# Kernel tuning notes

Measured on AMD Instinct MI355X. Metric: run time of the kernel, lower is better.

Reference implementation:

```python
import jax, jax.numpy as jnp
import numpy as np

B, N, C = 16, 2048, 80
CONF_THR = 0.2
NMS_THR = 0.45
OFFSET = 10000.0  # > max box coordinate, separates classes for batched per-class NMS


def setup_inputs() -> dict:
    key = jax.random.key(0)
    k1, k2, k3, k4 = jax.random.split(key, 4)
    cxcy = jax.random.uniform(k1, (B, N, 2)) * 640.0
    wh = jax.random.uniform(k2, (B, N, 2)) * 100.0 + 1.0
    boxes = jnp.concatenate([cxcy - wh / 2, cxcy + wh / 2], axis=-1)  # (x1,y1,x2,y2)
    scores = jax.random.uniform(k3, (B, N, 1))
    classprobs = jax.random.uniform(k4, (B, N, C))
    detection = jnp.concatenate([boxes, scores, classprobs], axis=-1)  # [B,N,85]
    return {"detection": detection}


def _iou_matrix(boxes):
    # boxes: [N,4] -> [N,N] pairwise IoU (torchvision convention, no +1)
    x1, y1, x2, y2 = boxes[:, 0], boxes[:, 1], boxes[:, 2], boxes[:, 3]
    area = jnp.clip(x2 - x1, 0.0) * jnp.clip(y2 - y1, 0.0)
    ix1 = jnp.maximum(x1[:, None], x1[None, :])
    iy1 = jnp.maximum(y1[:, None], y1[None, :])
    ix2 = jnp.minimum(x2[:, None], x2[None, :])
    iy2 = jnp.minimum(y2[:, None], y2[None, :])
    inter = jnp.clip(ix2 - ix1, 0.0) * jnp.clip(iy2 - iy1, 0.0)
    return inter / (area[:, None] + area[None, :] - inter + 1e-7)


def _filter_image(boxes, scores, classprobs, labels):
    # Confidence filter (target_class=None path)
    cand = scores > CONF_THR
    # Sort by descending score, non-candidates last (sort key is non-differentiable)
    sort_key = jnp.where(cand, scores, -jnp.inf)
    order = jnp.argsort(-jax.lax.stop_gradient(sort_key))
    b = boxes[order]
    s = scores[order]
    cp = classprobs[order]
    lb = labels[order]
    cd = cand[order]
    # Per-class NMS via coordinate offset: boxes of different classes never overlap
    ob = b + lb[:, None].astype(b.dtype) * OFFSET
    iou = _iou_matrix(ob)  # [N,N]
    idx = jnp.arange(N)

    def step(active, i):
        keep_i = active[i]
        active = active & ~(keep_i & (iou[i] > NMS_THR) & (idx > i))
        return active, keep_i

    _, keep = jax.lax.scan(step, cd, idx)
    # Final sort by descending score among kept boxes (max_predictions_per_image=-1)
    final_key = jnp.where(keep, jax.lax.stop_gradient(s), -jnp.inf)
    perm = jnp.argsort(-final_key)
    keep_p = keep[perm]
    m = keep_p.astype(b.dtype)
    out_boxes = b[perm] * m[:, None]
    out_scores = s[perm] * m
    out_classprobs = cp[perm] * m
    out_labels = jnp.where(keep_p, lb[perm], 0)
    return out_boxes, out_scores, out_classprobs, out_labels, keep_p


def reference(detection):
    # split_detections
    boxes = detection[..., :4]
    scores = detection[..., 4]
    cp_all = detection[..., 5:]
    classprobs = jnp.max(cp_all, axis=-1)
    labels = jnp.argmax(cp_all, axis=-1)
    ob, osc, ocp, olb, mask = jax.vmap(_filter_image)(boxes, scores, classprobs, labels)
    # Pack float outputs: [B, N, 6] = boxes(4) + score(1) + classprob(1); padded rows are zero
    out = jnp.concatenate([ob, osc[..., None], ocp[..., None]], axis=-1)
    return out, olb, mask
```

## Files before the change

### kernel.cpp

```cpp
#include <hip/hip_runtime.h>

#define BATCH 16
#define NBOX  2048
#define NCLS  80
#define ROWF  85
#define CONF_THRF 0.2f
#define CONF_BITS 0x3E4CCCCDu
#define NMS_THRF  0.45f
#define CAP   128
#define KCAP  64
#define JOBS  (BATCH*NCLS)

#define WS_SL   0
#define WS_CP   (WS_SL + (size_t)BATCH*NBOX*8)
#define WS_KC   (WS_CP + (size_t)BATCH*NBOX*4)
#define WS_KB   (WS_KC + (size_t)JOBS*KCAP*8)
#define WS_KCP  (WS_KB + (size_t)JOBS*KCAP*16)
#define WS_KCLS (WS_KCP + (size_t)JOBS*KCAP*4)

static __device__ inline unsigned long long shflx64(unsigned long long v, int m) {
  int lo = __shfl_xor((int)(unsigned)(v & 0xffffffffull), m, 64);
  int hi = __shfl_xor((int)(unsigned)(v >> 32), m, 64);
  return ((unsigned long long)(unsigned)hi << 32) | (unsigned)lo;
}

__global__ __launch_bounds__(256) void prep_kernel(const float* __restrict__ det,
                                                   unsigned long long* __restrict__ sl,
                                                   float* __restrict__ cp_ws,
                                                   float* __restrict__ outz) {
  const int tid = threadIdx.x;
  const int lane = tid & 63, wavei = tid >> 6;
  const int sub = lane & 15, grp = lane >> 4;
  const int row = blockIdx.x * 16 + wavei * 4 + grp;

  int gid = blockIdx.x * 256 + tid;
  if (gid < (BATCH * NBOX * 8) / 4)
    ((float4*)outz)[gid] = make_float4(0.f, 0.f, 0.f, 0.f);

  const float* r = det + (size_t)row * ROWF;
  float best = r[5 + sub];
  int bc = sub;
#pragma unroll
  for (int k = 1; k < 5; ++k) {
    float v = r[5 + sub + 16 * k];
    if (v > best) { best = v; bc = sub + 16 * k; }
  }
#pragma unroll
  for (int d = 1; d < 16; d <<= 1) {
    float ov = __shfl_xor(best, d, 16);
    int oc = __shfl_xor(bc, d, 16);
    if (ov > best || (ov == best && oc < bc)) { best = ov; bc = oc; }
  }
  if (sub == 0) {
    sl[row] = ((unsigned long long)__float_as_uint(r[4]) << 32) | (unsigned)bc;
    cp_ws[row] = best;
  }
}

__global__ __launch_bounds__(256) void nms16_kernel(const float* __restrict__ det,
                                                    const unsigned long long* __restrict__ sl,
                                                    const float* __restrict__ cp_ws,
                                                    unsigned long long* __restrict__ keptc,
                                                    float4* __restrict__ keptb,
                                                    float* __restrict__ keptcp,
                                                    int* __restrict__ kcls) {
  __shared__ unsigned short cand[4][CAP];
  const int tid = threadIdx.x;
  const int lane = tid & 63, wid = tid >> 6;
  const int j = blockIdx.x * 4 + wid;
  const int img = j / NCLS, c = j - img * NCLS;
  const size_t ibase = (size_t)img * NBOX;
  const unsigned long long* slImg = sl + ibase;
  unsigned short* mycand = cand[wid];

  unsigned mymask = 0;
#pragma unroll
  for (int it = 0; it < 32; ++it) {
    unsigned long long v = slImg[it * 64 + lane];
    bool match = ((unsigned)(v >> 32) > CONF_BITS) && ((unsigned)v == (unsigned)c);
    mymask |= (match ? 1u : 0u) << it;
  }
  int mycnt = __popc(mymask);
  int inc = mycnt;
#pragma unroll
  for (int d = 1; d < 64; d <<= 1) { int u = __shfl_up(inc, d, 64); if (lane >= d) inc += u; }
  int mybase = inc - mycnt;
  int total = __shfl(inc, 63, 64);
  int m = total < CAP ? total : CAP;
  {
    unsigned mk = mymask;
    int pos = mybase;
    while (mk) {
      int it = __ffs(mk) - 1; mk &= mk - 1;
      if (pos < CAP) mycand[pos] = (unsigned short)(it * 64 + lane);
      pos++;
    }
  }

  unsigned long long e0 = ~0ull, e1 = ~0ull;
  if (lane < m) {
    int n = mycand[lane];
    e0 = ((unsigned long long)(~(unsigned)(slImg[n] >> 32)) << 32) | (unsigned)n;
  }
  if (lane + 64 < m) {
    int n = mycand[lane + 64];
    e1 = ((unsigned long long)(~(unsigned)(slImg[n] >> 32)) << 32) | (unsigned)n;
  }
  const bool two = (m > 64);
  if (!two) {
#pragma unroll
    for (int k = 2; k <= 64; k <<= 1)
      for (int jj = k >> 1; jj > 0; jj >>= 1) {
        bool amLow = (lane & jj) == 0;
        bool up = ((lane & k) == 0);
        unsigned long long o = shflx64(e0, jj);
        e0 = (up == amLow) ? (e0 < o ? e0 : o) : (e0 > o ? e0 : o);
      }
  } else {
#pragma unroll
    for (int k = 2; k <= 128; k <<= 1)
      for (int jj = k >> 1; jj > 0; jj >>= 1) {
        if (jj == 64) {
          bool up = ((lane & k) == 0);
          if (up ? (e0 > e1) : (e0 < e1)) { unsigned long long t = e0; e0 = e1; e1 = t; }
        } else {
          bool amLow = (lane & jj) == 0;
          bool up0 = ((lane & k) == 0), up1 = (((lane + 64) & k) == 0);
          unsigned long long o0 = shflx64(e0, jj), o1 = shflx64(e1, jj);
          e0 = (up0 == amLow) ? (e0 < o0 ? e0 : o0) : (e0 > o0 ? e0 : o0);
          e1 = (up1 == amLow) ? (e1 < o1 ? e1 : o1) : (e1 > o1 ? e1 : o1);
        }
      }
  }

  const float off = (float)c * 10000.0f;
  bool valid0 = lane < m, valid1 = two && (lane + 64 < m);
  int n0 = (int)((unsigned)e0 & (NBOX - 1));
  int n1 = (int)((unsigned)e1 & (NBOX - 1));
  float a00 = 0, a01 = 0, a02 = 0, a03 = 0, cp0 = 0;
  float x1 = 0, y1 = 0, x2 = 0, y2 = 0, ar = 0;
  if (valid0) {
    const float* rr = det + (ibase + n0) * ROWF;
    a00 = rr[0]; a01 = rr[1]; a02 = rr[2]; a03 = rr[3];
    cp0 = cp_ws[ibase + n0];
    x1 = a00 + off; y1 = a01 + off; x2 = a02 + off; y2 = a03 + off;
    ar = fmaxf(x2 - x1, 0.0f) * fmaxf(y2 - y1, 0.0f);
  }
  float A10 = 0, A11 = 0, A12 = 0, A13 = 0, cp1 = 0;
  float X1 = 0, Y1 = 0, X2 = 0, Y2 = 0, AR = 0;
  if (valid1) {
    const float* rr = det + (ibase + n1) * ROWF;
    A10 = rr[0]; A11 = rr[1]; A12 = rr[2]; A13 = rr[3];
    cp1 = cp_ws[ibase + n1];
    X1 = A10 + off; Y1 = A11 + off; X2 = A12 + off; Y2 = A13 + off;
    AR = fmaxf(X2 - X1, 0.0f) * fmaxf(Y2 - Y1, 0.0f);
  }

  unsigned long long keptm0 = 0, und = __ballot(valid0);
  while (und) {
    int i = __ffsll((long long)und) - 1;
    keptm0 |= 1ull << i;
    float kx1 = __shfl(x1, i, 64), ky1 = __shfl(y1, i, 64);
    float kx2 = __shfl(x2, i, 64), ky2 = __shfl(y2, i, 64);
    float kar = __shfl(ar, i, 64);
    float iw = fminf(x2, kx2) - fmaxf(x1, kx1);
    float ih = fminf(y2, ky2) - fmaxf(y1, ky1);
    float inter = fmaxf(iw, 0.0f) * fmaxf(ih, 0.0f);
    float iou = inter / (((kar + ar) - inter) + 1e-7f);
    bool sup = (lane > i) && (iou > NMS_THRF);
    und &= ~__ballot(sup);
    und &= ~(1ull << i);
  }
  unsigned long long keptm1 = 0;
  if (two) {
    bool dead = false;
    unsigned long long km = keptm0;
    while (km) {
      int t = __ffsll((long long)km) - 1; km &= km - 1;
      float kx1 = __shfl(x1, t, 64), ky1 = __shfl(y1, t, 64);
      float kx2 = __shfl(x2, t, 64), ky2 = __shfl(y2, t, 64);
      float kar = __shfl(ar, t, 64);
      float iw = fminf(X2, kx2) - fmaxf(X1, kx1);
      float ih = fminf(Y2, ky2) - fmaxf(Y1, ky1);
      float inter = fmaxf(iw, 0.0f) * fmaxf(ih, 0.0f);
      float iou = inter / (((kar + AR) - inter) + 1e-7f);
      dead |= (iou > NMS_THRF);
    }
    unsigned long long und1 = __ballot(valid1 && !dead);
    while (und1) {
      int i = __ffsll((long long)und1) - 1;
      keptm1 |= 1ull << i;
      float kx1 = __shfl(X1, i, 64), ky1 = __shfl(Y1, i, 64);
      float kx2 = __shfl(X2, i, 64), ky2 = __shfl(Y2, i, 64);
      float kar = __shfl(AR, i, 64);
      float iw = fminf(X2, kx2) - fmaxf(X1, kx1);
      float ih = fminf(Y2, ky2) - fmaxf(Y1, ky1);
      float inter = fmaxf(iw, 0.0f) * fmaxf(ih, 0.0f);
      float iou = inter / (((kar + AR) - inter) + 1e-7f);
      bool sup = (lane > i) && (iou > NMS_THRF);
      und1 &= ~__ballot(sup);
      und1 &= ~(1ull << i);
    }
  }

  unsigned long long* dstk = keptc + (size_t)j * KCAP;
  float4* dstb = keptb + (size_t)j * KCAP;
  float* dstc = keptcp + (size_t)j * KCAP;
  if ((keptm0 >> lane) & 1) {
    int rank = __popcll(keptm0 & ((1ull << lane) - 1ull));
    if (rank < KCAP) {
      dstk[rank] = (e0 & 0xffffffff00000000ull) | (unsigned)((n0 << 7) | c);
      dstb[rank] = make_float4(a00, a01, a02, a03);
      dstc[rank] = cp0;
    }
  }
  if (two && ((keptm1 >> lane) & 1)) {
    int rank = __popcll(keptm0) + __popcll(keptm1 & ((1ull << lane) - 1ull));
    if (rank < KCAP) {
      dstk[rank] = (e1 & 0xffffffff00000000ull) | (unsigned)((n1 << 7) | c);
      dstb[rank] = make_float4(A10, A11, A12, A13);
      dstc[rank] = cp1;
    }
  }
  if (lane == 0) {
    int nk = __popcll(keptm0) + __popcll(keptm1);
    kcls[j] = nk < KCAP ? nk : KCAP;
  }
}

__global__ __launch_bounds__(1024) void outr_kernel(const float* __restrict__ cp_unused,
                                                    const unsigned long long* __restrict__ keptc,
                                                    const float4* __restrict__ keptb,
                                                    const float* __restrict__ keptcp,
                                                    const int* __restrict__ kcls,
                                                    float* __restrict__ out) {
  __shared__ unsigned long long keys[NBOX];
  __shared__ unsigned short srcmap[NBOX];
  __shared__ int offL[NCLS], cntL[NCLS];
  __shared__ int KtotS;
  const int img = blockIdx.x >> 5, seg = blockIdx.x & 31;
  const int tid = threadIdx.x;
  const int lane = tid & 63, wid = tid >> 6;
  const size_t ibase = (size_t)img * NBOX;

  if (wid == 0) {
    int v0 = kcls[img * NCLS + lane];
    int v1 = (lane < NCLS - 64) ? kcls[img * NCLS + 64 + lane] : 0;
    int s0 = v0;
#pragma unroll
    for (int d = 1; d < 64; d <<= 1) { int u = __shfl_up(s0, d, 64); if (lane >= d) s0 += u; }
    int total0 = __shfl(s0, 63, 64);
    int s1 = v1;
#pragma unroll
    for (int d = 1; d < 16; d <<= 1) { int u = __shfl_up(s1, d, 64); if (lane >= d) s1 += u; }
    offL[lane] = s0 - v0; cntL[lane] = v0;
    if (lane < NCLS - 64) { offL[64 + lane] = total0 + s1 - v1; cntL[64 + lane] = v1; }
    if (lane == 15) KtotS = total0 + s1;
  }
  __syncthreads();
  const int K = KtotS;
  if (seg * 64 >= K) return;

  {
    const int c = tid % NCLS;
    const int q0 = tid / NCLS;
    const int step = (c < (1024 - NCLS * (1024 / NCLS))) ? (1024 / NCLS + 1) : (1024 / NCLS);
    int kc = cntL[c], o = offL[c];
    const unsigned long long* srck = keptc + (size_t)(img * NCLS + c) * KCAP;
    for (int q = q0; q < kc; q += step) {
      keys[o + q] = srck[q];
      srcmap[o + q] = (unsigned short)(c * KCAP + q);
    }
  }
  __syncthreads();

  const int sbase = seg * 64 + (wid << 2);
  unsigned long long X[4];
  bool V[4];
#pragma unroll
  for (int q = 0; q < 4; ++q) {
    V[q] = (sbase + q) < K;
    X[q] = V[q] ? keys[sbase + q] : ~0ull;
  }

  const int bA = offL[lane], nA = cntL[lane];
  int bB = 0, nB = 0;
  if (lane < NCLS - 64) { bB = offL[64 + lane]; nB = cntL[64 + lane]; }
  int loA[4], hiA[4], loB[4], hiB[4];
#pragma unroll
  for (int q = 0; q < 4; ++q) {
    loA[q] = 0; hiA[q] = V[q] ? nA : 0;
    loB[q] = 0; hiB[q] = (lane < NCLS - 64 && V[q]) ? nB : 0;
  }
#pragma unroll
  for (int s = 0; s < 7; ++s) {
#pragma unroll
    for (int q = 0; q < 4; ++q) {
      if (loA[q] < hiA[q]) {
        int mid = (loA[q] + hiA[q]) >> 1;
        if (keys[bA + mid] < X[q]) loA[q] = mid + 1; else hiA[q] = mid;
      }
      if (loB[q] < hiB[q]) {
        int mid = (loB[q] + hiB[q]) >> 1;
        if (keys[bB + mid] < X[q]) loB[q] = mid + 1; else hiB[q] = mid;
      }
    }
  }
  int r[4];
#pragma unroll
  for (int q = 0; q < 4; ++q) {
    int v = loA[q] + loB[q];
#pragma unroll
    for (int d = 1; d < 64; d <<= 1) v += __shfl_xor(v, d, 64);
    r[q] = v;
  }

  if (lane < 4 && V[lane]) {
    unsigned long long xm = (lane == 0) ? X[0] : (lane == 1) ? X[1] : (lane == 2) ? X[2] : X[3];
    int rm = (lane == 0) ? r[0] : (lane == 1) ? r[1] : (lane == 2) ? r[2] : r[3];
    int sm = srcmap[sbase + lane];
    int lb = (unsigned)xm & 127;
    const size_t rec = (size_t)img * NCLS * KCAP + sm;
    float4 b = keptb[rec];
    float cp = keptcp[rec];
    float* orow = out + (ibase + rm) * 6;
    orow[0] = b.x; orow[1] = b.y; orow[2] = b.z; orow[3] = b.w;
    orow[4] = __uint_as_float(~(unsigned)(xm >> 32));
    orow[5] = cp;
    out[(size_t)BATCH * NBOX * 6 + ibase + rm] = (float)lb;
    out[(size_t)BATCH * NBOX * 7 + ibase + rm] = 1.0f;
  }
}

extern "C" void kernel_launch(void* const* d_in, const int* in_sizes, int n_in,
                              void* d_out, int out_size, void* d_ws, size_t ws_size,
                              hipStream_t stream) {
  const float* det = (const float*)d_in[0];
  float* out = (float*)d_out;
  char* ws = (char*)d_ws;

  unsigned long long* sl = (unsigned long long*)(ws + WS_SL);
  float* cp_ws = (float*)(ws + WS_CP);
  unsigned long long* keptc = (unsigned long long*)(ws + WS_KC);
  float4* keptb = (float4*)(ws + WS_KB);
  float* keptcp = (float*)(ws + WS_KCP);
  int* kcls = (int*)(ws + WS_KCLS);

  prep_kernel<<<BATCH * NBOX / 16, 256, 0, stream>>>(det, sl, cp_ws, out);
  nms16_kernel<<<JOBS / 4, 256, 0, stream>>>(det, sl, cp_ws, keptc, keptb, keptcp, kcls);
  outr_kernel<<<BATCH * 32, 1024, 0, stream>>>(cp_ws, keptc, keptb, keptcp, kcls, out);
}
```

Baseline: 32.22 us.

## Rank kept boxes per class pair without compacting keys or prefix scan

The output-ranking kernel now copies the whole per-class kept-key array (80×64) into shared memory directly. This drops the prefix-scan and compaction pass and the srcmap indirection. Each block handles two classes (40 blocks per image) instead of 64-element segments of the compacted list, and each wave ranks 8 elements with binary search over all class lists. The aim is to remove a barrier and the scattered compaction, at the cost of always loading 40 KB of keys per block and having blocks with empty class pairs exit after that load.

Result: slower. 44.05 us (+36.7%).

```diff
diff --git a/kernel.cpp b/kernel.cpp
--- a/kernel.cpp
+++ b/kernel.cpp
@@ -228,107 +228,91 @@
   }
 }
 
-__global__ __launch_bounds__(1024) void outr_kernel(const float* __restrict__ cp_unused,
-                                                    const unsigned long long* __restrict__ keptc,
-                                                    const float4* __restrict__ keptb,
-                                                    const float* __restrict__ keptcp,
-                                                    const int* __restrict__ kcls,
-                                                    float* __restrict__ out) {
-  __shared__ unsigned long long keys[NBOX];
-  __shared__ unsigned short srcmap[NBOX];
-  __shared__ int offL[NCLS], cntL[NCLS];
-  __shared__ int KtotS;
-  const int img = blockIdx.x >> 5, seg = blockIdx.x & 31;
+__global__ __launch_bounds__(1024) void outr3_kernel(const unsigned long long* __restrict__ keptc,
+                                                     const float4* __restrict__ keptb,
+                                                     const float* __restrict__ keptcp,
+                                                     const int* __restrict__ kcls,
+                                                     float* __restrict__ out) {
+  __shared__ unsigned long long keys[NCLS * KCAP];
+  __shared__ int cntL[NCLS];
+  const int img = blockIdx.x / 40, seg = blockIdx.x % 40;
   const int tid = threadIdx.x;
   const int lane = tid & 63, wid = tid >> 6;
   const size_t ibase = (size_t)img * NBOX;
 
-  if (wid == 0) {
-    int v0 = kcls[img * NCLS + lane];
-    int v1 = (lane < NCLS - 64) ? kcls[img * NCLS + 64 + lane] : 0;
-    int s0 = v0;
-#pragma unroll
-    for (int d = 1; d < 64; d <<= 1) { int u = __shfl_up(s0, d, 64); if (lane >= d) s0 += u; }
-    int total0 = __shfl(s0, 63, 64);
-    int s1 = v1;
-#pragma unroll
-    for (int d = 1; d < 16; d <<= 1) { int u = __shfl_up(s1, d, 64); if (lane >= d) s1 += u; }
-    offL[lane] = s0 - v0; cntL[lane] = v0;
-    if (lane < NCLS - 64) { offL[64 + lane] = total0 + s1 - v1; cntL[64 + lane] = v1; }
-    if (lane == 15) KtotS = total0 + s1;
-  }
+  {
+    const unsigned long long* src = keptc + (size_t)img * NCLS * KCAP;
+#pragma unroll
+    for (int i = 0; i < 5; ++i) keys[tid + i * 1024] = src[tid + i * 1024];
+  }
+  if (tid < NCLS) cntL[tid] = kcls[img * NCLS + tid];
   __syncthreads();
-  const int K = KtotS;
-  if (seg * 64 >= K) return;
-
-  {
-    const int c = tid % NCLS;
-    const int q0 = tid / NCLS;
-    const int step = (c < (1024 - NCLS * (1024 / NCLS))) ? (1024 / NCLS + 1) : (1024 / NCLS);
-    int kc = cntL[c], o = offL[c];
-    const unsigned long long* srck = keptc + (size_t)(img * NCLS + c) * KCAP;
-    for (int q = q0; q < kc; q += step) {
-      keys[o + q] = srck[q];
-      srcmap[o + q] = (unsigned short)(c * KCAP + q);
-    }
-  }
-  __syncthreads();
-
-  const int sbase = seg * 64 + (wid << 2);
-  unsigned long long X[4];
-  bool V[4];
-#pragma unroll
-  for (int q = 0; q < 4; ++q) {
-    V[q] = (sbase + q) < K;
-    X[q] = V[q] ? keys[sbase + q] : ~0ull;
-  }
-
-  const int bA = offL[lane], nA = cntL[lane];
+
+  const int c0 = seg * 2, c1 = seg * 2 + 1;
+  const int n0 = cntL[c0], n1 = cntL[c1];
+  const int ntot = n0 + n1;
+  if (ntot == 0) return;
+
+  unsigned long long X[8];
+  bool V[8];
+  int CC[8], QQ[8];
+#pragma unroll
+  for (int s = 0; s < 8; ++s) {
+    int e = wid + s * 16;
+    V[s] = e < ntot;
+    int cc = (e < n0) ? c0 : c1;
+    int qq = (e < n0) ? e : e - n0;
+    CC[s] = cc; QQ[s] = qq;
+    X[s] = V[s] ? keys[cc * KCAP + qq] : ~0ull;
+  }
+
+  const int bA = lane * KCAP, nA = cntL[lane];
   int bB = 0, nB = 0;
-  if (lane < NCLS - 64) { bB = offL[64 + lane]; nB = cntL[64 + lane]; }
-  int loA[4], hiA[4], loB[4], hiB[4];
-#pragma unroll
-  for (int q = 0; q < 4; ++q) {
-    loA[q] = 0; hiA[q] = V[q] ? nA : 0;
-    loB[q] = 0; hiB[q] = (lane < NCLS - 64 && V[q]) ? nB : 0;
-  }
-#pragma unroll
-  for (int s = 0; s < 7; ++s) {
-#pragma unroll
-    for (int q = 0; q < 4; ++q) {
-      if (loA[q] < hiA[q]) {
-        int mid = (loA[q] + hiA[q]) >> 1;
-        if (keys[bA + mid] < X[q]) loA[q] = mid + 1; else hiA[q] = mid;
+  if (lane < NCLS - 64) { bB = (64 + lane) * KCAP; nB = cntL[64 + lane]; }
+  int loA[8], hiA[8], loB[8], hiB[8];
+#pragma unroll
+  for (int s = 0; s < 8; ++s) {
+    loA[s] = 0; hiA[s] = V[s] ? nA : 0;
+    loB[s] = 0; hiB[s] = (lane < NCLS - 64 && V[s]) ? nB : 0;
+  }
+#pragma unroll
+  for (int st = 0; st < 6; ++st) {
+#pragma unroll
+    for (int s = 0; s < 8; ++s) {
+      if (loA[s] < hiA[s]) {
+        int mid = (loA[s] + hiA[s]) >> 1;
+        if (keys[bA + mid] < X[s]) loA[s] = mid + 1; else hiA[s] = mid;
       }
-      if (loB[q] < hiB[q]) {
-        int mid = (loB[q] + hiB[q]) >> 1;
-        if (keys[bB + mid] < X[q]) loB[q] = mid + 1; else hiB[q] = mid;
+      if (loB[s] < hiB[s]) {
+        int mid = (loB[s] + hiB[s]) >> 1;
+        if (keys[bB + mid] < X[s]) loB[s] = mid + 1; else hiB[s] = mid;
       }
     }
   }
-  int r[4];
-#pragma unroll
-  for (int q = 0; q < 4; ++q) {
-    int v = loA[q] + loB[q];
+  int r[8];
+#pragma unroll
+  for (int s = 0; s < 8; ++s) {
+    int v = loA[s] + loB[s];
 #pragma unroll
     for (int d = 1; d < 64; d <<= 1) v += __shfl_xor(v, d, 64);
-    r[q] = v;
-  }
-
-  if (lane < 4 && V[lane]) {
-    unsigned long long xm = (lane == 0) ? X[0] : (lane == 1) ? X[1] : (lane == 2) ? X[2] : X[3];
-    int rm = (lane == 0) ? r[0] : (lane == 1) ? r[1] : (lane == 2) ? r[2] : r[3];
-    int sm = srcmap[sbase + lane];
-    int lb = (unsigned)xm & 127;
-    const size_t rec = (size_t)img * NCLS * KCAP + sm;
-    float4 b = keptb[rec];
-    float cp = keptcp[rec];
-    float* orow = out + (ibase + rm) * 6;
-    orow[0] = b.x; orow[1] = b.y; orow[2] = b.z; orow[3] = b.w;
-    orow[4] = __uint_as_float(~(unsigned)(xm >> 32));
-    orow[5] = cp;
-    out[(size_t)BATCH * NBOX * 6 + ibase + rm] = (float)lb;
-    out[(size_t)BATCH * NBOX * 7 + ibase + rm] = 1.0f;
+    r[s] = v;
+  }
+
+#pragma unroll
+  for (int s = 0; s < 8; ++s) {
+    if (lane == s && V[s] && r[s] < NBOX) {
+      const size_t rec = (size_t)img * NCLS * KCAP + CC[s] * KCAP + QQ[s];
+      float4 b = keptb[rec];
+      float cp = keptcp[rec];
+      unsigned long long xm = X[s];
+      int rm = r[s];
+      float* orow = out + (ibase + rm) * 6;
+      orow[0] = b.x; orow[1] = b.y; orow[2] = b.z; orow[3] = b.w;
+      orow[4] = __uint_as_float(~(unsigned)(xm >> 32));
+      orow[5] = cp;
+      out[(size_t)BATCH * NBOX * 6 + ibase + rm] = (float)((unsigned)xm & 127);
+      out[(size_t)BATCH * NBOX * 7 + ibase + rm] = 1.0f;
+    }
   }
 }
 
@@ -348,5 +332,5 @@
 
   prep_kernel<<<BATCH * NBOX / 16, 256, 0, stream>>>(det, sl, cp_ws, out);
   nms16_kernel<<<JOBS / 4, 256, 0, stream>>>(det, sl, cp_ws, keptc, keptb, keptcp, kcls);
-  outr_kernel<<<BATCH * 32, 1024, 0, stream>>>(cp_ws, keptc, keptb, keptcp, kcls, out);
-}
+  outr3_kernel<<<BATCH * 40, 1024, 0, stream>>>(keptc, keptb, keptcp, kcls, out);
+}
```
